# Kernel tuning notes

Measured on AMD Instinct MI355X. Metric: run time of the kernel, lower is better.

## Reference

```python
import jax, jax.numpy as jnp
import numpy as np

B, F, H, D, K = 16384, 4096, 512, 64, 512  # batch, feat, hidden, emb_dim, codebook size
M = H // D  # code positions per sample


def _leaky(h):
    return jnp.where(h > 0, h, 0.01 * h)


def setup_inputs() -> dict:
    key = jax.random.key(0)
    ks = jax.random.split(key, 16)
    lin = lambda k, i, o: jax.random.normal(k, (i, o), jnp.float32) * (1.0 / np.sqrt(i))
    return {
        "x": jax.random.uniform(ks[0], (B, F), jnp.float32),
        "We1": lin(ks[1], F, 256), "be1": jnp.zeros((256,), jnp.float32),
        "We2": lin(ks[2], 256, 128), "be2": jnp.zeros((128,), jnp.float32),
        "We3": lin(ks[3], 128, H), "be3": jnp.zeros((H,), jnp.float32),
        "Wd1": lin(ks[4], H, 128), "bd1": jnp.zeros((128,), jnp.float32),
        "Wd2": lin(ks[5], 128, 256), "bd2": jnp.zeros((256,), jnp.float32),
        "Wd3": lin(ks[6], 256, F), "bd3": jnp.zeros((F,), jnp.float32),
        "codebook": jax.random.normal(ks[7], (D, K), jnp.float32) * 0.02,  # (emb_dim, num_embeddings)
    }


def _nearest(z_e, codebook):
    # z_e: (B, D, M); codebook: (D, K). Squared-distance argmin over K.
    x2 = jnp.sum(z_e * z_e, axis=1)                       # (B, M)
    xw = jnp.einsum('bdm,dk->bmk', z_e, codebook)         # (B, M, K)
    w2 = jnp.sum(codebook * codebook, axis=0)             # (K,)
    idx = jnp.argmin(x2[..., None] - 2.0 * xw + w2, axis=-1)  # (B, M)
    quant = jnp.swapaxes(codebook.T[idx], 1, 2)           # (B, D, M)
    return quant, idx


def reference(x, We1, be1, We2, be2, We3, be3, Wd1, bd1, Wd2, bd2, Wd3, bd3, codebook):
    # encoder MLP
    h = _leaky(x @ We1 + be1)
    h = _leaky(h @ We2 + be2)
    h = _leaky(h @ We3 + be3)                             # (B, H)
    z_e = h.reshape(B, D, M)
    # emb(z_e, weight_sg=True): straight-through, weight detached
    quant_sg, idx = _nearest(z_e, jax.lax.stop_gradient(codebook))
    z_q = z_e + jax.lax.stop_gradient(quant_sg - z_e)
    # emb(z_e.detach()): grads (if any) flow to codebook via gather
    emb, _ = _nearest(jax.lax.stop_gradient(z_e), codebook)
    # decoder MLP
    g = _leaky(z_q.reshape(B, H) @ Wd1 + bd1)
    g = _leaky(g @ Wd2 + bd2)
    X_pred = jax.nn.sigmoid(g @ Wd3 + bd3)                # (B, F)
    return idx, z_e, z_q, emb, X_pred
```

## Files before the change

kernel.cpp:

```cpp
#include <hip/hip_runtime.h>
#include <cstdint>
#include <cstddef>


static constexpr int BB = 16384;
static constexpr int TM = 128, TN = 128, TK = 16;

typedef __attribute__((ext_vector_type(8))) short short8;
typedef __attribute__((ext_vector_type(8))) _Float16 half8;
typedef __attribute__((ext_vector_type(4))) float f32x4;

__device__ __forceinline__ unsigned short f2bf(float f) {
    union { float f; uint32_t u; } v; v.f = f;
    uint32_t r = (v.u + 0x7FFFu + ((v.u >> 16) & 1u)) >> 16;
    return (unsigned short)r;
}

__device__ __forceinline__ int bsw(int c) { return c + ((c >> 5) << 2); }

#define GLL16(gp, lp) \
    __builtin_amdgcn_global_load_lds( \
        (const __attribute__((address_space(1))) uint32_t*)(gp), \
        (__attribute__((address_space(3))) uint32_t*)(lp), 16, 0, 0)

__global__ __launch_bounds__(256) void gemm_fp32(
    const float* __restrict__ A, const float* __restrict__ Bm,
    const float* __restrict__ bias, float* __restrict__ C,
    float* __restrict__ part,
    int M, int N, int Kd, int kLen, int act)
{
    __shared__ float As[TK][TM + 4];
    __shared__ float Bs[TK][140];
    const int tid = threadIdx.x;
    const int bm = blockIdx.y * TM;
    const int bn = blockIdx.x * TN;
    const int kStart = blockIdx.z * kLen;
    const int tx = tid & 15;
    const int ty = tid >> 4;

    const int arow = tid >> 2;
    const int acol = (tid & 3) << 2;
    const int brow = tid >> 5;
    const int bcol = (tid & 31) << 2;

    float acc[8][8];
#pragma unroll
    for (int i = 0; i < 8; i++)
#pragma unroll
        for (int j = 0; j < 8; j++) acc[i][j] = 0.f;

    const float* Ap0 = A + (size_t)(bm + arow) * Kd + acol;
    const float* Ap1 = A + (size_t)(bm + arow + 64) * Kd + acol;
    const float* Bp0 = Bm + (size_t)brow * N + bn + bcol;
    const float* Bp1 = Bm + (size_t)(brow + 8) * N + bn + bcol;

    const int pb0 = bsw(bcol);
    const int prb0 = bsw(tx * 8);
    const int prb1 = prb0 + 4;

    for (int k0 = kStart; k0 < kStart + kLen; k0 += TK) {
        const float4 a0 = *(const float4*)(Ap0 + k0);
        const float4 a1 = *(const float4*)(Ap1 + k0);
        const float4 b0 = *(const float4*)(Bp0 + (size_t)k0 * N);
        const float4 b1 = *(const float4*)(Bp1 + (size_t)k0 * N);
        __syncthreads();
        As[acol + 0][arow] = a0.x; As[acol + 1][arow] = a0.y;
        As[acol + 2][arow] = a0.z; As[acol + 3][arow] = a0.w;
        As[acol + 0][arow + 64] = a1.x; As[acol + 1][arow + 64] = a1.y;
        As[acol + 2][arow + 64] = a1.z; As[acol + 3][arow + 64] = a1.w;
        *(float4*)&Bs[brow][pb0]     = b0;
        *(float4*)&Bs[brow + 8][pb0] = b1;
        __syncthreads();
#pragma unroll
        for (int kk = 0; kk < TK; kk++) {
            float a[8], b[8];
            *(float4*)&a[0] = *(const float4*)&As[kk][ty * 8];
            *(float4*)&a[4] = *(const float4*)&As[kk][ty * 8 + 4];
            *(float4*)&b[0] = *(const float4*)&Bs[kk][prb0];
            *(float4*)&b[4] = *(const float4*)&Bs[kk][prb1];
#pragma unroll
            for (int i = 0; i < 8; i++)
#pragma unroll
                for (int j = 0; j < 8; j++)
                    acc[i][j] = fmaf(a[i], b[j], acc[i][j]);
        }
    }

    if (part) {
        float* P = part + (size_t)blockIdx.z * M * N;
#pragma unroll
        for (int i = 0; i < 8; i++) {
            const int row = bm + ty * 8 + i;
            *(float4*)&P[(size_t)row * N + bn + tx * 8]     = *(float4*)&acc[i][0];
            *(float4*)&P[(size_t)row * N + bn + tx * 8 + 4] = *(float4*)&acc[i][4];
        }
        return;
    }

    float bv[8];
#pragma unroll
    for (int j = 0; j < 8; j++) bv[j] = bias[bn + tx * 8 + j];
#pragma unroll
    for (int i = 0; i < 8; i++) {
        const int row = bm + ty * 8 + i;
        float o[8];
#pragma unroll
        for (int j = 0; j < 8; j++) {
            float v = acc[i][j] + bv[j];
            if (act == 0) v = (v > 0.f) ? v : 0.01f * v;
            else          v = 1.0f / (1.0f + __expf(-v));
            o[j] = v;
        }
        *(float4*)&C[(size_t)row * N + bn + tx * 8]     = *(float4*)&o[0];
        *(float4*)&C[(size_t)row * N + bn + tx * 8 + 4] = *(float4*)&o[4];
    }
}

__global__ __launch_bounds__(256) void combine_act(
    const float* __restrict__ part, int S, size_t MN,
    const float* __restrict__ bias, int N,
    float* __restrict__ outF, unsigned short* __restrict__ outB)
{
    const size_t e = ((size_t)blockIdx.x * 256 + threadIdx.x) * 4;
    if (e >= MN) return;
    float4 s = *(const float4*)(part + e);
    for (int i = 1; i < S; i++) {
        const float4 p = *(const float4*)(part + (size_t)i * MN + e);
        s.x += p.x; s.y += p.y; s.z += p.z; s.w += p.w;
    }
    const int col = (int)(e & (size_t)(N - 1));
    const float4 bv = *(const float4*)(bias + col);
    float v0 = s.x + bv.x, v1 = s.y + bv.y, v2 = s.z + bv.z, v3 = s.w + bv.w;
    v0 = (v0 > 0.f) ? v0 : 0.01f * v0;
    v1 = (v1 > 0.f) ? v1 : 0.01f * v1;
    v2 = (v2 > 0.f) ? v2 : 0.01f * v2;
    v3 = (v3 > 0.f) ? v3 : 0.01f * v3;
    if (outF) {
        float4 o; o.x = v0; o.y = v1; o.z = v2; o.w = v3;
        *(float4*)(outF + e) = o;
    } else {
        ushort4 o; o.x = f2bf(v0); o.y = f2bf(v1); o.z = f2bf(v2); o.w = f2bf(v3);
        *(ushort4*)(outB + e) = o;
    }
}

__global__ __launch_bounds__(256) void transpose_cast(
    const float* __restrict__ W, unsigned short* __restrict__ WT, int R, int Cc)
{
    __shared__ float s[32][33];
    const int tx = threadIdx.x & 31, ty = threadIdx.x >> 5;
    const int c0 = blockIdx.x * 32, r0 = blockIdx.y * 32;
#pragma unroll
    for (int i = 0; i < 4; i++)
        s[ty + i * 8][tx] = W[(size_t)(r0 + ty + i * 8) * Cc + c0 + tx];
    __syncthreads();
#pragma unroll
    for (int i = 0; i < 4; i++)
        WT[(size_t)(c0 + ty + i * 8) * R + r0 + tx] = f2bf(s[tx][ty + i * 8]);
}

__global__ __launch_bounds__(256) void transpose_split_f16(
    const float* __restrict__ W, unsigned short* __restrict__ Th,
    unsigned short* __restrict__ Tl, int R, int Cc)
{
    __shared__ float s[32][33];
    const int tx = threadIdx.x & 31, ty = threadIdx.x >> 5;
    const int c0 = blockIdx.x * 32, r0 = blockIdx.y * 32;
#pragma unroll
    for (int i = 0; i < 4; i++)
        s[ty + i * 8][tx] = W[(size_t)(r0 + ty + i * 8) * Cc + c0 + tx];
    __syncthreads();
#pragma unroll
    for (int i = 0; i < 4; i++) {
        const float f = s[tx][ty + i * 8];
        const _Float16 h = (_Float16)f;
        const float fh = (float)h;
        const _Float16 lo = (_Float16)((f - fh) * 4096.0f);
        union { _Float16 hf; unsigned short u; } ch, cl;
        ch.hf = h; cl.hf = lo;
        Th[(size_t)(c0 + ty + i * 8) * R + r0 + tx] = ch.u;
        Tl[(size_t)(c0 + ty + i * 8) * R + r0 + tx] = cl.u;
    }
}

__global__ __launch_bounds__(256, 2) void gemm_f16x2_enc1(
    const float* __restrict__ X,
    const unsigned short* __restrict__ Bh,
    const unsigned short* __restrict__ Bl,
    float* __restrict__ part)
{
    __shared__ short Ah[2][2048];
    __shared__ short Al[2][2048];
    __shared__ short Bhs[2][8192];
    __shared__ short Bls[2][8192];
    const int tid = threadIdx.x;
    const int l = tid & 63, w = tid >> 6;
    const int lm = l & 15, lq = l >> 4;
    const int bm = blockIdx.y * 64;
    const int kStart = blockIdx.z * 2048;

    const float* gA = X + (size_t)(bm + w * 16 + lm) * 4096 + kStart + lq * 8;
    const unsigned short* gBh0 = Bh + (size_t)(w * 64 + lm) * 4096 + kStart + lq * 8;
    const unsigned short* gBl0 = Bl + (size_t)(w * 64 + lm) * 4096 + kStart + lq * 8;
    const size_t rstep = (size_t)16 * 4096;

    const int aoff = (w << 9) + (l << 3);
    const int fr0 = (lq << 7) + (lm << 3);
    const int bfrB = (w << 11);

    f32x4 acc1[4][4], acc2[4][4];
#pragma unroll
    for (int i = 0; i < 4; i++)
#pragma unroll
        for (int j = 0; j < 4; j++) {
            acc1[i][j] = (f32x4){0.f, 0.f, 0.f, 0.f};
            acc2[i][j] = (f32x4){0.f, 0.f, 0.f, 0.f};
        }

    {
        float fv[8];
        *(float4*)&fv[0] = *(const float4*)(gA);
        *(float4*)&fv[4] = *(const float4*)(gA + 4);
        GLL16(gBh0,             &Bhs[0][bfrB]);
        GLL16(gBh0 + rstep,     &Bhs[0][bfrB + 512]);
        GLL16(gBh0 + 2 * rstep, &Bhs[0][bfrB + 1024]);
        GLL16(gBh0 + 3 * rstep, &Bhs[0][bfrB + 1536]);
        GLL16(gBl0,             &Bls[0][bfrB]);
        GLL16(gBl0 + rstep,     &Bls[0][bfrB + 512]);
        GLL16(gBl0 + 2 * rstep, &Bls[0][bfrB + 1024]);
        GLL16(gBl0 + 3 * rstep, &Bls[0][bfrB + 1536]);
        union { _Float16 h[8]; short8 s; } uh, ul;
#pragma unroll
        for (int e = 0; e < 8; e++) {
            const float f = fv[e];
            const _Float16 h = (_Float16)f;
            const float fh = (float)h;
            uh.h[e] = h;
            ul.h[e] = (_Float16)((f - fh) * 4096.0f);
        }
        *(short8*)&Ah[0][aoff] = uh.s;
        *(short8*)&Al[0][aoff] = ul.s;
    }

    for (int k0 = 0; k0 < 2048; k0 += 32) {
        const int buf = (k0 >> 5) & 1;
        const int nb = buf ^ 1;
        const int kn = k0 + 32;
        __syncthreads();
        float4 a0, a1;
        if (kn < 2048) {
            a0 = *(const float4*)(gA + kn);
            a1 = *(const float4*)(gA + kn + 4);
            GLL16(gBh0 + kn,             &Bhs[nb][bfrB]);
            GLL16(gBh0 + kn + rstep,     &Bhs[nb][bfrB + 512]);
            GLL16(gBh0 + kn + 2 * rstep, &Bhs[nb][bfrB + 1024]);
            GLL16(gBh0 + kn + 3 * rstep, &Bhs[nb][bfrB + 1536]);
            GLL16(gBl0 + kn,             &Bls[nb][bfrB]);
            GLL16(gBl0 + kn + rstep,     &Bls[nb][bfrB + 512]);
            GLL16(gBl0 + kn + 2 * rstep, &Bls[nb][bfrB + 1024]);
            GLL16(gBl0 + kn + 3 * rstep, &Bls[nb][bfrB + 1536]);
        }
        half8 ah[4], bh[4];
#pragma unroll
        for (int i = 0; i < 4; i++)
            ah[i] = *(const half8*)&Ah[buf][(i << 9) + fr0];
#pragma unroll
        for (int j = 0; j < 4; j++)
            bh[j] = *(const half8*)&Bhs[buf][bfrB + (j << 9) + fr0];
#pragma unroll
        for (int i = 0; i < 4; i++)
#pragma unroll
            for (int j = 0; j < 4; j++)
                acc1[i][j] = __builtin_amdgcn_mfma_f32_16x16x32_f16(
                    ah[i], bh[j], acc1[i][j], 0, 0, 0);
        half8 bl[4];
#pragma unroll
        for (int j = 0; j < 4; j++)
            bl[j] = *(const half8*)&Bls[buf][bfrB + (j << 9) + fr0];
#pragma unroll
        for (int i = 0; i < 4; i++)
#pragma unroll
            for (int j = 0; j < 4; j++)
                acc2[i][j] = __builtin_amdgcn_mfma_f32_16x16x32_f16(
                    ah[i], bl[j], acc2[i][j], 0, 0, 0);
        half8 al[4];
#pragma unroll
        for (int i = 0; i < 4; i++)
            al[i] = *(const half8*)&Al[buf][(i << 9) + fr0];
#pragma unroll
        for (int i = 0; i < 4; i++)
#pragma unroll
            for (int j = 0; j < 4; j++)
                acc2[i][j] = __builtin_amdgcn_mfma_f32_16x16x32_f16(
                    al[i], bh[j], acc2[i][j], 0, 0, 0);
        if (kn < 2048) {
            float fv[8];
            *(float4*)&fv[0] = a0;
            *(float4*)&fv[4] = a1;
            union { _Float16 h[8]; short8 s; } uh, ul;
#pragma unroll
            for (int e = 0; e < 8; e++) {
                const float f = fv[e];
                const _Float16 h = (_Float16)f;
                const float fh = (float)h;
                uh.h[e] = h;
                ul.h[e] = (_Float16)((f - fh) * 4096.0f);
            }
            *(short8*)&Ah[nb][aoff] = uh.s;
            *(short8*)&Al[nb][aoff] = ul.s;
        }
    }

    float* P = part + (size_t)blockIdx.z * BB * 256;
    const float inv = 0.000244140625f;
#pragma unroll
    for (int i = 0; i < 4; i++)
#pragma unroll
        for (int j = 0; j < 4; j++) {
            const int col = w * 64 + j * 16 + lm;
#pragma unroll
            for (int r = 0; r < 4; r++) {
                const int row = bm + i * 16 + lq * 4 + r;
                P[(size_t)row * 256 + col] = acc1[i][j][r] + inv * acc2[i][j][r];
            }
        }
}

__global__ __launch_bounds__(256) void gemm_bf16_dec3(
    const unsigned short* __restrict__ Ag,
    const unsigned short* __restrict__ Bt,
    const float* __restrict__ bias, float* __restrict__ C)
{
    __shared__ short As[4096];
    __shared__ short Bs2[4096];
    const int tid = threadIdx.x;
    const int l = tid & 63, w = tid >> 6;
    const int lm = l & 15, lq = l >> 4;
    const int bm = blockIdx.y * 128, bn = blockIdx.x * 128;
    const int wm = (w >> 1) * 64, wn = (w & 1) * 64;

    const int t0 = w * 2, t1 = w * 2 + 1;
    const unsigned short* ga0 = Ag + (size_t)(bm + t0 * 16 + lm) * 256 + lq * 8;
    const unsigned short* ga1 = Ag + (size_t)(bm + t1 * 16 + lm) * 256 + lq * 8;
    const unsigned short* gb0 = Bt + (size_t)(bn + t0 * 16 + lm) * 256 + lq * 8;
    const unsigned short* gb1 = Bt + (size_t)(bn + t1 * 16 + lm) * 256 + lq * 8;

    f32x4 acc[4][4];
#pragma unroll
    for (int i = 0; i < 4; i++)
#pragma unroll
        for (int j = 0; j < 4; j++) acc[i][j] = (f32x4){0.f, 0.f, 0.f, 0.f};

    for (int k0 = 0; k0 < 256; k0 += 32) {
        __syncthreads();
        GLL16(ga0 + k0, &As[t0 * 512]);
        GLL16(ga1 + k0, &As[t1 * 512]);
        GLL16(gb0 + k0, &Bs2[t0 * 512]);
        GLL16(gb1 + k0, &Bs2[t1 * 512]);
        __syncthreads();
        short8 af[4], bf[4];
#pragma unroll
        for (int i = 0; i < 4; i++)
            af[i] = *(const short8*)&As[((w >> 1) * 4 + i) * 512 + lq * 128 + lm * 8];
#pragma unroll
        for (int j = 0; j < 4; j++)
            bf[j] = *(const short8*)&Bs2[((w & 1) * 4 + j) * 512 + lq * 128 + lm * 8];
#pragma unroll
        for (int i = 0; i < 4; i++)
#pragma unroll
            for (int j = 0; j < 4; j++)
                acc[i][j] = __builtin_amdgcn_mfma_f32_16x16x32_bf16(
                    af[i], bf[j], acc[i][j], 0, 0, 0);
    }

#pragma unroll
    for (int i = 0; i < 4; i++) {
#pragma unroll
        for (int j = 0; j < 4; j++) {
            const int col = bn + wn + j * 16 + lm;
            const float bv = bias[col];
#pragma unroll
            for (int r = 0; r < 4; r++) {
                const int row = bm + wm + i * 16 + lq * 4 + r;
                float v = acc[i][j][r] + bv;
                v = 1.0f / (1.0f + __expf(-v));
                C[(size_t)row * 4096 + col] = v;
            }
        }
    }
}

__global__ __launch_bounds__(512) void vq_argmin(
    const float* __restrict__ ze, const float* __restrict__ cb,
    float* __restrict__ idxf)
{
    __shared__ float cbs[64 * 512];
    __shared__ float As[64][68];
    __shared__ float w2s[512];
    const int tid = threadIdx.x;
    const int p0 = blockIdx.x * 64;

    const float4* cb4 = (const float4*)cb;
    float4* cbs4 = (float4*)cbs;
    for (int i = tid; i < 8192; i += 512) cbs4[i] = cb4[i];

    const float4* ze4 = (const float4*)(ze + (size_t)p0 * 64);
    for (int i = tid; i < 1024; i += 512) {
        float4 v = ze4[i];
        int e = i * 4;
        int bo = e >> 9, r = e & 511;
        int d = r >> 3, m = r & 7;
        *(float4*)&As[d][bo * 8 + m] = v;
    }
    __syncthreads();

    {
        float s = 0.f;
#pragma unroll
        for (int d = 0; d < 64; ++d) { float c = cbs[d * 512 + tid]; s = fmaf(c, c, s); }
        w2s[tid] = s;
    }
    __syncthreads();

    const int tx = tid & 63;
    const int ty = tid >> 6;

    float acc[8][8], x2a[8];
#pragma unroll
    for (int i = 0; i < 8; i++) {
        x2a[i] = 0.f;
#pragma unroll
        for (int j = 0; j < 8; j++) acc[i][j] = 0.f;
    }

#pragma unroll 8
    for (int kk = 0; kk < 64; ++kk) {
        float a[8], b[8];
        *(float4*)&a[0] = *(const float4*)&As[kk][ty * 8];
        *(float4*)&a[4] = *(const float4*)&As[kk][ty * 8 + 4];
        *(float4*)&b[0] = *(const float4*)&cbs[kk * 512 + tx * 8];
        *(float4*)&b[4] = *(const float4*)&cbs[kk * 512 + tx * 8 + 4];
#pragma unroll
        for (int i = 0; i < 8; i++) x2a[i] = fmaf(a[i], a[i], x2a[i]);
#pragma unroll
        for (int i = 0; i < 8; i++)
#pragma unroll
            for (int j = 0; j < 8; j++)
                acc[i][j] = fmaf(a[i], b[j], acc[i][j]);
    }

    float w2v[8];
#pragma unroll
    for (int j = 0; j < 8; j++) w2v[j] = w2s[tx * 8 + j];

#pragma unroll
    for (int i = 0; i < 8; i++) {
        float bd = 3.4e38f; int bk = 1 << 30;
#pragma unroll
        for (int j = 0; j < 8; j++) {
            float dsc = (x2a[i] - 2.0f * acc[i][j]) + w2v[j];
            if (dsc < bd) { bd = dsc; bk = tx * 8 + j; }
        }
        for (int off = 32; off > 0; off >>= 1) {
            float od = __shfl_xor(bd, off);
            int   ok = __shfl_xor(bk, off);
            if (od < bd || (od == bd && ok < bk)) { bd = od; bk = ok; }
        }
        if (tx == i) idxf[p0 + ty * 8 + i] = (float)bk;
    }
}

__global__ __launch_bounds__(256) void vq_gather(
    const float* __restrict__ ze, const float* __restrict__ idxf,
    const float* __restrict__ cb,
    float* __restrict__ zq, float* __restrict__ emb)
{
    const int t = blockIdx.x * 256 + threadIdx.x;
    const int e = t * 4;
    const int b = e >> 9, r = e & 511;
    const int d = r >> 3, m = r & 7;
    const float4 z = *(const float4*)(ze + e);
    float q[4];
#pragma unroll
    for (int c = 0; c < 4; c++) {
        int k = (int)idxf[b * 8 + m + c];
        q[c] = cb[d * 512 + k];
    }
    float4 zq4, em4;
    zq4.x = z.x + (q[0] - z.x); zq4.y = z.y + (q[1] - z.y);
    zq4.z = z.z + (q[2] - z.z); zq4.w = z.w + (q[3] - z.w);
    em4.x = q[0]; em4.y = q[1]; em4.z = q[2]; em4.w = q[3];
    *(float4*)(zq + e) = zq4;
    *(float4*)(emb + e) = em4;
}

extern "C" void kernel_launch(void* const* d_in, const int* in_sizes, int n_in,
                              void* d_out, int out_size, void* d_ws, size_t ws_size,
                              hipStream_t stream)
{
    const float* x   = (const float*)d_in[0];
    const float* We1 = (const float*)d_in[1];
    const float* be1 = (const float*)d_in[2];
    const float* We2 = (const float*)d_in[3];
    const float* be2 = (const float*)d_in[4];
    const float* We3 = (const float*)d_in[5];
    const float* be3 = (const float*)d_in[6];
    const float* Wd1 = (const float*)d_in[7];
    const float* bd1 = (const float*)d_in[8];
    const float* Wd2 = (const float*)d_in[9];
    const float* bd2 = (const float*)d_in[10];
    const float* Wd3 = (const float*)d_in[11];
    const float* bd3 = (const float*)d_in[12];
    const float* cb  = (const float*)d_in[13];

    float* out   = (float*)d_out;
    float* o_idx = out;
    float* o_ze  = o_idx + 131072;
    float* o_zq  = o_ze + 8388608;
    float* o_emb = o_zq + 8388608;
    float* o_X   = o_emb + 8388608;

    float* h1 = (float*)d_ws;
    float* h2 = h1 + (size_t)BB * 256;
    float* g1 = h1;
    unsigned short* g2b = (unsigned short*)(h1 + (size_t)BB * 128);
    unsigned short* WT  = (unsigned short*)h2;

    unsigned short* Bth = (unsigned short*)(o_X + 16777216);
    unsigned short* Btl = Bth + 1048576;

    transpose_split_f16<<<dim3(8, 128), 256, 0, stream>>>(We1, Bth, Btl, 4096, 256);
    gemm_f16x2_enc1<<<dim3(1, 256, 2), 256, 0, stream>>>(x, Bth, Btl, o_X);
    combine_act<<<4096, 256, 0, stream>>>(o_X, 2, (size_t)BB * 256, be1, 256, h1, nullptr);
    gemm_fp32<<<dim3(1, 128, 2), 256, 0, stream>>>(
        h1, We2, nullptr, nullptr, o_X, BB, 128, 256, 128, 0);
    combine_act<<<2048, 256, 0, stream>>>(o_X, 2, (size_t)BB * 128, be2, 128, h2, nullptr);
    gemm_fp32<<<dim3(4, 128, 1), 256, 0, stream>>>(
        h2, We3, be3, o_ze, nullptr, BB, 512, 128, 128, 0);

    vq_argmin<<<dim3(2048), dim3(512), 0, stream>>>(o_ze, cb, o_idx);
    vq_gather<<<dim3(8192), dim3(256), 0, stream>>>(o_ze, o_idx, cb, o_zq, o_emb);

    transpose_cast<<<dim3(128, 8), 256, 0, stream>>>(Wd3, WT, 256, 4096);

    gemm_fp32<<<dim3(1, 128, 4), 256, 0, stream>>>(
        o_zq, Wd1, nullptr, nullptr, o_X, BB, 128, 512, 128, 0);
    combine_act<<<2048, 256, 0, stream>>>(o_X, 4, (size_t)BB * 128, bd1, 128, g1, nullptr);
    gemm_fp32<<<dim3(2, 128, 2), 256, 0, stream>>>(
        g1, Wd2, nullptr, nullptr, o_X, BB, 256, 128, 64, 0);
    combine_act<<<4096, 256, 0, stream>>>(o_X, 2, (size_t)BB * 256, bd2, 256, nullptr, g2b);
    gemm_bf16_dec3<<<dim3(32, 128), 256, 0, stream>>>(g2b, WT, bd3, o_X);
}
```

Baseline: 1.095 ms.

## Load encoder weight fragments directly from global into registers, bypassing LDS

In the first encoder GEMM, the B (weight hi/lo) tiles are no longer staged through double-buffered shared memory via global_load_lds. Each wave now loads its own weight fragments straight from global memory into registers every k-step. The X activation loads also become nontemporal loads. This cuts LDS use, which may raise occupancy, and removes LDS round trips for B. In exchange, the weight loads are no longer prefetched one stage ahead, so global latency now sits on the MFMA critical path.

```diff
diff --git a/kernel.cpp b/kernel.cpp
--- a/kernel.cpp
+++ b/kernel.cpp
@@ -191,8 +191,6 @@
 {
     __shared__ short Ah[2][2048];
     __shared__ short Al[2][2048];
-    __shared__ short Bhs[2][8192];
-    __shared__ short Bls[2][8192];
     const int tid = threadIdx.x;
     const int l = tid & 63, w = tid >> 6;
     const int lm = l & 15, lq = l >> 4;
@@ -200,13 +198,12 @@
     const int kStart = blockIdx.z * 2048;
 
     const float* gA = X + (size_t)(bm + w * 16 + lm) * 4096 + kStart + lq * 8;
-    const unsigned short* gBh0 = Bh + (size_t)(w * 64 + lm) * 4096 + kStart + lq * 8;
-    const unsigned short* gBl0 = Bl + (size_t)(w * 64 + lm) * 4096 + kStart + lq * 8;
+    const unsigned short* gBh = Bh + (size_t)(w * 64 + lm) * 4096 + kStart + lq * 8;
+    const unsigned short* gBl = Bl + (size_t)(w * 64 + lm) * 4096 + kStart + lq * 8;
     const size_t rstep = (size_t)16 * 4096;
 
     const int aoff = (w << 9) + (l << 3);
     const int fr0 = (lq << 7) + (lm << 3);
-    const int bfrB = (w << 11);
 
     f32x4 acc1[4][4], acc2[4][4];
 #pragma unroll
@@ -219,16 +216,8 @@
 
     {
         float fv[8];
-        *(float4*)&fv[0] = *(const float4*)(gA);
-        *(float4*)&fv[4] = *(const float4*)(gA + 4);
-        GLL16(gBh0,             &Bhs[0][bfrB]);
-        GLL16(gBh0 + rstep,     &Bhs[0][bfrB + 512]);
-        GLL16(gBh0 + 2 * rstep, &Bhs[0][bfrB + 1024]);
-        GLL16(gBh0 + 3 * rstep, &Bhs[0][bfrB + 1536]);
-        GLL16(gBl0,             &Bls[0][bfrB]);
-        GLL16(gBl0 + rstep,     &Bls[0][bfrB + 512]);
-        GLL16(gBl0 + 2 * rstep, &Bls[0][bfrB + 1024]);
-        GLL16(gBl0 + 3 * rstep, &Bls[0][bfrB + 1536]);
+        *(f32x4*)&fv[0] = __builtin_nontemporal_load((const f32x4*)(gA));
+        *(f32x4*)&fv[4] = __builtin_nontemporal_load((const f32x4*)(gA + 4));
         union { _Float16 h[8]; short8 s; } uh, ul;
 #pragma unroll
         for (int e = 0; e < 8; e++) {
@@ -247,36 +236,27 @@
         const int nb = buf ^ 1;
         const int kn = k0 + 32;
         __syncthreads();
-        float4 a0, a1;
+        half8 bh[4], bl[4];
+#pragma unroll
+        for (int j = 0; j < 4; j++) {
+            bh[j] = *(const half8*)(gBh + (size_t)j * rstep + k0);
+            bl[j] = *(const half8*)(gBl + (size_t)j * rstep + k0);
+        }
+        f32x4 a0, a1;
         if (kn < 2048) {
-            a0 = *(const float4*)(gA + kn);
-            a1 = *(const float4*)(gA + kn + 4);
-            GLL16(gBh0 + kn,             &Bhs[nb][bfrB]);
-            GLL16(gBh0 + kn + rstep,     &Bhs[nb][bfrB + 512]);
-            GLL16(gBh0 + kn + 2 * rstep, &Bhs[nb][bfrB + 1024]);
-            GLL16(gBh0 + kn + 3 * rstep, &Bhs[nb][bfrB + 1536]);
-            GLL16(gBl0 + kn,             &Bls[nb][bfrB]);
-            GLL16(gBl0 + kn + rstep,     &Bls[nb][bfrB + 512]);
-            GLL16(gBl0 + kn + 2 * rstep, &Bls[nb][bfrB + 1024]);
-            GLL16(gBl0 + kn + 3 * rstep, &Bls[nb][bfrB + 1536]);
-        }
-        half8 ah[4], bh[4];
+            a0 = __builtin_nontemporal_load((const f32x4*)(gA + kn));
+            a1 = __builtin_nontemporal_load((const f32x4*)(gA + kn + 4));
+        }
+        half8 ah[4];
 #pragma unroll
         for (int i = 0; i < 4; i++)
             ah[i] = *(const half8*)&Ah[buf][(i << 9) + fr0];
-#pragma unroll
-        for (int j = 0; j < 4; j++)
-            bh[j] = *(const half8*)&Bhs[buf][bfrB + (j << 9) + fr0];
 #pragma unroll
         for (int i = 0; i < 4; i++)
 #pragma unroll
             for (int j = 0; j < 4; j++)
                 acc1[i][j] = __builtin_amdgcn_mfma_f32_16x16x32_f16(
                     ah[i], bh[j], acc1[i][j], 0, 0, 0);
-        half8 bl[4];
-#pragma unroll
-        for (int j = 0; j < 4; j++)
-            bl[j] = *(const half8*)&Bls[buf][bfrB + (j << 9) + fr0];
 #pragma unroll
         for (int i = 0; i < 4; i++)
 #pragma unroll
@@ -295,8 +275,8 @@
                     al[i], bh[j], acc2[i][j], 0, 0, 0);
         if (kn < 2048) {
             float fv[8];
-            *(float4*)&fv[0] = a0;
-            *(float4*)&fv[4] = a1;
+            *(f32x4*)&fv[0] = a0;
+            *(f32x4*)&fv[4] = a1;
             union { _Float16 h[8]; short8 s; } uh, ul;
 #pragma unroll
             for (int e = 0; e < 8; e++) {
```

New measurement: 1.080 ms. About the same (-1.4%).
